# Kernel optimization log

Hardware: AMD Instinct MI355X
Metric: run time of the kernel (lower is better)

## Reference

```python
import jax, jax.numpy as jnp
import numpy as np

B, S, HID, USZ, PSZ, OUT = 128, 512, 768, 200, 200, 200
N_SENT = 16  # 16 sentences of 32 tokens; offsets row = [0,32,...,480,-1]


def setup_inputs() -> dict:
    key = jax.random.key(0)
    ks = jax.random.split(key, 8)
    H = jax.random.normal(ks[0], (B, S, HID), jnp.float32)
    u = jax.random.normal(ks[1], (B, USZ), jnp.float32)
    p = jax.random.normal(ks[2], (B, PSZ), jnp.float32)
    Wh = jax.random.normal(ks[3], (HID, OUT), jnp.float32) * 0.05
    Wu = jax.random.normal(ks[4], (USZ, OUT), jnp.float32) * 0.05
    Wp = jax.random.normal(ks[5], (PSZ, OUT), jnp.float32) * 0.05
    v = jax.random.normal(ks[6], (OUT,), jnp.float32) * 0.05
    b = jnp.zeros((OUT,), jnp.float32)  # torch buffer self.b = zeros
    # offsets: N_SENT sentence starts + trailing -1 sentinel -> [B, N_SENT+1]
    row = jnp.concatenate([jnp.arange(N_SENT, dtype=jnp.int32) * (S // N_SENT),
                           jnp.array([-1], jnp.int32)])
    sentence_offsets = jnp.tile(row[None, :], (B, 1))
    return {"H": H, "u": u, "p": p, "Wh": Wh, "Wu": Wu, "Wp": Wp,
            "v": v, "b": b, "sentence_offsets": sentence_offsets}


def reference(H, u, p, Wh, Wu, Wp, v, b, sentence_offsets):
    # Additive attention scores for every token: v . tanh(Wh H + Wu u + Wp p + b)
    Ht = jnp.einsum('bsh,ho->bso', H, Wh)                      # [B,S,OUT]
    ut = (u @ Wu)[:, None, :]                                  # [B,1,OUT]
    pt = (p @ Wp)[:, None, :]                                  # [B,1,OUT]
    scores = jnp.tanh(Ht + ut + pt + b) @ v                    # [B,S]

    Bsz, Sl, _ = H.shape
    beg = sentence_offsets[:, :-1]                             # [B,M]
    nxt = sentence_offsets[:, 1:]                              # [B,M]
    valid = beg != -1
    # faithful to torch: end = 512 if next==-1 else next-1 (off-by-one kept)
    end = jnp.where(nxt == -1, Sl, nxt - 1)
    t = jnp.arange(Sl)
    mask = valid[:, :, None] & (t[None, None, :] >= beg[:, :, None]) \
           & (t[None, None, :] < end[:, :, None])              # [B,M,S]

    neg_inf = jnp.float32(-jnp.inf)
    em = jnp.where(mask, scores[:, None, :], neg_inf)
    m = jnp.max(em, axis=-1, keepdims=True)
    w = jnp.exp(em - jnp.where(jnp.isfinite(m), m, 0.0)) * mask
    denom = jnp.sum(w, axis=-1, keepdims=True)
    alphas = w / jnp.where(denom > 0, denom, 1.0)              # ragged softmax
    # per-sentence weighted sum of H -> [B, M, HID] (invalid sentences = 0)
    return jnp.einsum('bms,bsh->bmh', alphas, H)
```

## Files before the change

kernel.cpp:

```cpp
#include <hip/hip_runtime.h>
#include <hip/hip_bf16.h>
#include <math.h>

#define Bn   128
#define Sn   512
#define HIDn 768
#define OUTn 200
#define MSEG 16
#define NPAD 208
#define NT   13

typedef __attribute__((ext_vector_type(8))) short short8;
typedef __attribute__((ext_vector_type(4))) float f32x4;

static __device__ inline unsigned short f2bf(float f) {
  union { float f; unsigned u; } v; v.f = f;
  unsigned r = v.u + 0x7FFFu + ((v.u >> 16) & 1u);
  return (unsigned short)(r >> 16);
}

static __device__ inline float fast_tanh(float x) {
  float t = fabsf(x);
  float e = __expf(-2.f * t);
  float r = (1.f - e) * __builtin_amdgcn_rcpf(1.f + e);
  return copysignf(r, x);
}

__global__ __launch_bounds__(256) void setup_kernel(
    const float* __restrict__ Wh, const float* __restrict__ v,
    unsigned short* __restrict__ WhT, float* __restrict__ vP) {
  __shared__ float tile[16][17];
  int n0 = (blockIdx.x % 13) * 16;
  int k0 = (blockIdx.x / 13) * 16;
  int tid = threadIdx.x;
  if (blockIdx.x == 0 && tid < NPAD) vP[tid] = (tid < OUTn) ? v[tid] : 0.f;
  int tk = tid >> 4, tn = tid & 15;
  float val = 0.f;
  int n = n0 + tn;
  if (n < OUTn) val = Wh[(size_t)(k0 + tk) * OUTn + n];
  tile[tk][tn] = val;
  __syncthreads();
  int tn2 = tid >> 4, tk2 = tid & 15;
  WhT[(size_t)(n0 + tn2) * HIDn + k0 + tk2] = f2bf(tile[tk2][tn2]);
}

__global__ __launch_bounds__(256) void bias_kernel(
    const float* __restrict__ u, const float* __restrict__ p,
    const float* __restrict__ Wu, const float* __restrict__ Wp,
    const float* __restrict__ bvec, float* __restrict__ biasP) {
  int b = blockIdx.x;
  __shared__ float ul[OUTn], pl[OUTn];
  int tid = threadIdx.x;
  if (tid < OUTn) { ul[tid] = u[b * OUTn + tid]; pl[tid] = p[b * OUTn + tid]; }
  __syncthreads();
  if (tid < NPAD) {
    float s0 = 0.f, s1 = 0.f;
    if (tid < OUTn) {
      s0 = bvec[tid];
      for (int k = 0; k < OUTn; k += 2) {
        s0 += ul[k] * Wu[k * OUTn + tid] + pl[k] * Wp[k * OUTn + tid];
        s1 += ul[k + 1] * Wu[(k + 1) * OUTn + tid] + pl[k + 1] * Wp[(k + 1) * OUTn + tid];
      }
    }
    biasP[(size_t)b * NPAD + tid] = s0 + s1;
  }
}

__global__ __launch_bounds__(256) void fused_kernel(
    const float* __restrict__ H, const unsigned short* __restrict__ WhT,
    const float* __restrict__ biasP, const float* __restrict__ vP,
    const int* __restrict__ offs, float* __restrict__ out) {
  __shared__ float al[128];
  int tid = threadIdx.x, wave = tid >> 6, lane = tid & 63;
  int quad = lane >> 4, l16 = lane & 15;
  int m0 = blockIdx.x * 128;
  int b = m0 >> 9;
  int s0 = m0 & 511;

  f32x4 acc[2][NT];
  for (int mt = 0; mt < 2; ++mt)
    for (int nt = 0; nt < NT; ++nt) acc[mt][nt] = (f32x4){0.f, 0.f, 0.f, 0.f};

  const float* Abase = H + (size_t)(m0 + wave * 32 + l16) * HIDn + quad * 8;
  const unsigned short* Bbase = WhT + (size_t)l16 * HIDn + quad * 8;

  for (int k0 = 0; k0 < HIDn; k0 += 32) {
    float4 f[2][2];
#pragma unroll
    for (int mt = 0; mt < 2; ++mt) {
      const float* ap = Abase + (size_t)mt * 16 * HIDn + k0;
      f[mt][0] = *(const float4*)ap;
      f[mt][1] = *(const float4*)(ap + 4);
    }
    short8 bfr[NT];
#pragma unroll
    for (int nt = 0; nt < NT; ++nt)
      bfr[nt] = *(const short8*)(Bbase + (size_t)nt * 16 * HIDn + k0);

    short8 a[2];
#pragma unroll
    for (int mt = 0; mt < 2; ++mt) {
      short8 t;
      t[0] = f2bf(f[mt][0].x); t[1] = f2bf(f[mt][0].y);
      t[2] = f2bf(f[mt][0].z); t[3] = f2bf(f[mt][0].w);
      t[4] = f2bf(f[mt][1].x); t[5] = f2bf(f[mt][1].y);
      t[6] = f2bf(f[mt][1].z); t[7] = f2bf(f[mt][1].w);
      a[mt] = t;
    }
#pragma unroll
    for (int nt = 0; nt < NT; ++nt) {
      acc[0][nt] = __builtin_amdgcn_mfma_f32_16x16x32_bf16(a[0], bfr[nt], acc[0][nt], 0, 0, 0);
      acc[1][nt] = __builtin_amdgcn_mfma_f32_16x16x32_bf16(a[1], bfr[nt], acc[1][nt], 0, 0, 0);
    }
  }

  const float* bp = biasP + (size_t)b * NPAD;
  float sc[2][4];
#pragma unroll
  for (int mt = 0; mt < 2; ++mt) {
#pragma unroll
    for (int r = 0; r < 4; ++r) {
      float s = 0.f;
#pragma unroll
      for (int nt = 0; nt < NT; ++nt) {
        int n = nt * 16 + l16;
        s += fast_tanh(acc[mt][nt][r] + bp[n]) * vP[n];
      }
      s += __shfl_xor(s, 1); s += __shfl_xor(s, 2);
      s += __shfl_xor(s, 4); s += __shfl_xor(s, 8);
      sc[mt][r] = s;
    }
  }

  int seg = (s0 >> 5) + wave;
  int beg = offs[b * (MSEG + 1) + seg];
  int nxt = offs[b * (MSEG + 1) + seg + 1];
  bool valid = (beg != -1);
  int end = (nxt == -1) ? Sn : nxt - 1;

  float x[2][4];
  float mx = -INFINITY;
#pragma unroll
  for (int mt = 0; mt < 2; ++mt)
#pragma unroll
    for (int r = 0; r < 4; ++r) {
      int row = s0 + wave * 32 + mt * 16 + quad * 4 + r;
      bool in = valid && row >= beg && row < end;
      x[mt][r] = in ? sc[mt][r] : -INFINITY;
      mx = fmaxf(mx, x[mt][r]);
    }
  mx = fmaxf(mx, __shfl_xor(mx, 16));
  mx = fmaxf(mx, __shfl_xor(mx, 32));
  float mm = (mx > -1e30f) ? mx : 0.f;

  float e[2][4], ls = 0.f;
#pragma unroll
  for (int mt = 0; mt < 2; ++mt)
#pragma unroll
    for (int r = 0; r < 4; ++r) {
      e[mt][r] = __expf(x[mt][r] - mm);
      ls += e[mt][r];
    }
  ls += __shfl_xor(ls, 16);
  ls += __shfl_xor(ls, 32);
  float inv = (ls > 0.f) ? 1.f / ls : 0.f;

  if (l16 == 0) {
#pragma unroll
    for (int mt = 0; mt < 2; ++mt)
#pragma unroll
      for (int r = 0; r < 4; ++r)
        al[wave * 32 + mt * 16 + quad * 4 + r] = e[mt][r] * inv;
  }

  const float4* Hrow = (const float4*)(H + (size_t)(b * Sn + s0 + wave * 32) * HIDn);
  float4 o0 = {0,0,0,0}, o1 = {0,0,0,0}, o2 = {0,0,0,0};
  for (int i = 0; i < 32; ++i) {
    float a = al[wave * 32 + i];
    if (a != 0.f) {
      const float4* hp = Hrow + (size_t)i * (HIDn / 4);
      float4 h0 = hp[lane], h1 = hp[lane + 64], h2 = hp[lane + 128];
      o0.x += a * h0.x; o0.y += a * h0.y; o0.z += a * h0.z; o0.w += a * h0.w;
      o1.x += a * h1.x; o1.y += a * h1.y; o1.z += a * h1.z; o1.w += a * h1.w;
      o2.x += a * h2.x; o2.y += a * h2.y; o2.z += a * h2.z; o2.w += a * h2.w;
    }
  }
  float4* op = (float4*)(out + ((size_t)b * MSEG + seg) * HIDn);
  op[lane] = o0; op[lane + 64] = o1; op[lane + 128] = o2;
}

extern "C" void kernel_launch(void* const* d_in, const int* in_sizes, int n_in,
                              void* d_out, int out_size, void* d_ws, size_t ws_size,
                              hipStream_t stream) {
  const float* H    = (const float*)d_in[0];
  const float* u    = (const float*)d_in[1];
  const float* p    = (const float*)d_in[2];
  const float* Wh   = (const float*)d_in[3];
  const float* Wu   = (const float*)d_in[4];
  const float* Wp   = (const float*)d_in[5];
  const float* v    = (const float*)d_in[6];
  const float* bvec = (const float*)d_in[7];
  const int*   offs = (const int*)d_in[8];
  float* out = (float*)d_out;

  float* biasP = (float*)d_ws;
  float* vP    = biasP + (size_t)Bn * NPAD;
  unsigned short* WhT = (unsigned short*)(vP + NPAD);

  setup_kernel<<<13 * 48, 256, 0, stream>>>(Wh, v, WhT, vP);
  bias_kernel<<<Bn, 256, 0, stream>>>(u, p, Wu, Wp, bvec, biasP);
  fused_kernel<<<(Bn * Sn) / 128, 256, 0, stream>>>(H, WhT, biasP, vP, offs, out);
}
```

Before: 383.9 us.

## Pre-swizzle Wh into MFMA fragment order and double-buffer H loads

The setup kernel now writes Wh in bf16 directly in MFMA B-fragment order, so each lane reads one contiguous short8 per tile and the wave's loads are fully coalesced instead of strided. The main GEMM loop is fully unrolled and prefetches the next K-slice of H into a second register buffer while the current slice is converted and multiplied. Launch bounds now request 2 blocks per SM. The extra buffers and full unrolling raise register pressure, which could cause spills or limit occupancy.

```diff
diff --git a/kernel.cpp b/kernel.cpp
--- a/kernel.cpp
+++ b/kernel.cpp
@@ -9,6 +9,7 @@
 #define MSEG 16
 #define NPAD 208
 #define NT   13
+#define KIT  (HIDn / 32)
 
 typedef __attribute__((ext_vector_type(8))) short short8;
 typedef __attribute__((ext_vector_type(4))) float f32x4;
@@ -28,20 +29,18 @@
 
 __global__ __launch_bounds__(256) void setup_kernel(
     const float* __restrict__ Wh, const float* __restrict__ v,
-    unsigned short* __restrict__ WhT, float* __restrict__ vP) {
-  __shared__ float tile[16][17];
-  int n0 = (blockIdx.x % 13) * 16;
-  int k0 = (blockIdx.x / 13) * 16;
-  int tid = threadIdx.x;
-  if (blockIdx.x == 0 && tid < NPAD) vP[tid] = (tid < OUTn) ? v[tid] : 0.f;
-  int tk = tid >> 4, tn = tid & 15;
-  float val = 0.f;
-  int n = n0 + tn;
-  if (n < OUTn) val = Wh[(size_t)(k0 + tk) * OUTn + n];
-  tile[tk][tn] = val;
-  __syncthreads();
-  int tn2 = tid >> 4, tk2 = tid & 15;
-  WhT[(size_t)(n0 + tn2) * HIDn + k0 + tk2] = f2bf(tile[tk2][tn2]);
+    unsigned short* __restrict__ WhF, float* __restrict__ vP) {
+  int idx = blockIdx.x * 256 + threadIdx.x;
+  if (blockIdx.x == 0 && threadIdx.x < NPAD)
+    vP[threadIdx.x] = (threadIdx.x < OUTn) ? v[threadIdx.x] : 0.f;
+  if (idx < NPAD * HIDn) {
+    int n = idx / HIDn;
+    int k = idx - n * HIDn;
+    float val = (n < OUTn) ? Wh[(size_t)k * OUTn + n] : 0.f;
+    size_t d = ((size_t)(k >> 5) * NT + (n >> 4)) * 512
+             + ((k >> 3) & 3) * 128 + (n & 15) * 8 + (k & 7);
+    WhF[d] = f2bf(val);
+  }
 }
 
 __global__ __launch_bounds__(256) void bias_kernel(
@@ -66,8 +65,8 @@
   }
 }
 
-__global__ __launch_bounds__(256) void fused_kernel(
-    const float* __restrict__ H, const unsigned short* __restrict__ WhT,
+__global__ __launch_bounds__(256, 2) void fused_kernel(
+    const float* __restrict__ H, const unsigned short* __restrict__ WhF,
     const float* __restrict__ biasP, const float* __restrict__ vP,
     const int* __restrict__ offs, float* __restrict__ out) {
   __shared__ float al[128];
@@ -82,29 +81,40 @@
     for (int nt = 0; nt < NT; ++nt) acc[mt][nt] = (f32x4){0.f, 0.f, 0.f, 0.f};
 
   const float* Abase = H + (size_t)(m0 + wave * 32 + l16) * HIDn + quad * 8;
-  const unsigned short* Bbase = WhT + (size_t)l16 * HIDn + quad * 8;
-
-  for (int k0 = 0; k0 < HIDn; k0 += 32) {
-    float4 f[2][2];
-#pragma unroll
-    for (int mt = 0; mt < 2; ++mt) {
-      const float* ap = Abase + (size_t)mt * 16 * HIDn + k0;
-      f[mt][0] = *(const float4*)ap;
-      f[mt][1] = *(const float4*)(ap + 4);
+  const short8* Bw = (const short8*)WhF + lane;
+
+  float4 f[2][2][2];
+#pragma unroll
+  for (int mt = 0; mt < 2; ++mt) {
+    const float* ap = Abase + (size_t)mt * 16 * HIDn;
+    f[0][mt][0] = *(const float4*)ap;
+    f[0][mt][1] = *(const float4*)(ap + 4);
+  }
+
+#pragma unroll
+  for (int it = 0; it < KIT; ++it) {
+    int cur = it & 1;
+    if (it + 1 < KIT) {
+#pragma unroll
+      for (int mt = 0; mt < 2; ++mt) {
+        const float* ap = Abase + (size_t)mt * 16 * HIDn + (it + 1) * 32;
+        f[1 - cur][mt][0] = *(const float4*)ap;
+        f[1 - cur][mt][1] = *(const float4*)(ap + 4);
+      }
     }
     short8 bfr[NT];
 #pragma unroll
     for (int nt = 0; nt < NT; ++nt)
-      bfr[nt] = *(const short8*)(Bbase + (size_t)nt * 16 * HIDn + k0);
+      bfr[nt] = Bw[(it * NT + nt) * 64];
 
     short8 a[2];
 #pragma unroll
     for (int mt = 0; mt < 2; ++mt) {
       short8 t;
-      t[0] = f2bf(f[mt][0].x); t[1] = f2bf(f[mt][0].y);
-      t[2] = f2bf(f[mt][0].z); t[3] = f2bf(f[mt][0].w);
-      t[4] = f2bf(f[mt][1].x); t[5] = f2bf(f[mt][1].y);
-      t[6] = f2bf(f[mt][1].z); t[7] = f2bf(f[mt][1].w);
+      t[0] = f2bf(f[cur][mt][0].x); t[1] = f2bf(f[cur][mt][0].y);
+      t[2] = f2bf(f[cur][mt][0].z); t[3] = f2bf(f[cur][mt][0].w);
+      t[4] = f2bf(f[cur][mt][1].x); t[5] = f2bf(f[cur][mt][1].y);
+      t[6] = f2bf(f[cur][mt][1].z); t[7] = f2bf(f[cur][mt][1].w);
       a[mt] = t;
     }
 #pragma unroll
@@ -205,9 +215,9 @@
 
   float* biasP = (float*)d_ws;
   float* vP    = biasP + (size_t)Bn * NPAD;
-  unsigned short* WhT = (unsigned short*)(vP + NPAD);
-
-  setup_kernel<<<13 * 48, 256, 0, stream>>>(Wh, v, WhT, vP);
+  unsigned short* WhF = (unsigned short*)(vP + NPAD);
+
+  setup_kernel<<<(NPAD * HIDn + 255) / 256, 256, 0, stream>>>(Wh, v, WhF, vP);
   bias_kernel<<<Bn, 256, 0, stream>>>(u, p, Wu, Wp, bvec, biasP);
-  fused_kernel<<<(Bn * Sn) / 128, 256, 0, stream>>>(H, WhT, biasP, vP, offs, out);
-}
+  fused_kernel<<<(Bn * Sn) / 128, 256, 0, stream>>>(H, WhF, biasP, vP, offs, out);
+}
```

Measured after the change: 359.4 us. 1.07x faster.
